# Optimization experiments

Measured on AMD Instinct MI355X. Metric: run time of the kernel, lower is better.

The kernel has to match this reference:

```python
import jax, jax.numpy as jnp
import numpy as np

N_NODES = 50000
N_EDGES = 300000
F_IN = 11
D = 256


def _gcn_conv(h, src, dst, deg_inv_sqrt, W, b, n):
    """PyG GCNConv: out = D^{-1/2} (A + I) D^{-1/2} (h W) + b.
    src/dst already include self-loops; deg_inv_sqrt precomputed."""
    norm = deg_inv_sqrt[src] * deg_inv_sqrt[dst]          # [E+N]
    hw = h @ W                                            # [N, D]
    msg = hw[src] * norm[:, None]                         # [E+N, D]
    out = jax.ops.segment_sum(msg, dst, num_segments=n)   # [N, D]
    return out + b


def setup_inputs() -> dict:
    key = jax.random.key(0)
    ks = jax.random.split(key, 8)
    x = jax.random.normal(ks[0], (N_NODES, F_IN), dtype=jnp.float32)
    edge_index = jax.random.randint(ks[1], (2, N_EDGES), 0, N_NODES, dtype=jnp.int32)
    s = 0.05
    W_embed = jax.random.normal(ks[2], (F_IN, D), dtype=jnp.float32) * s
    b_embed = jnp.zeros((D,), dtype=jnp.float32)
    W1 = jax.random.normal(ks[3], (D, D), dtype=jnp.float32) * s
    b1 = jnp.zeros((D,), dtype=jnp.float32)
    W2 = jax.random.normal(ks[4], (D, D), dtype=jnp.float32) * s
    b2 = jnp.zeros((D,), dtype=jnp.float32)
    return {"x": x, "edge_index": edge_index, "W_embed": W_embed, "b_embed": b_embed,
            "W1": W1, "b1": b1, "W2": W2, "b2": b2}


def reference(x, edge_index, W_embed, b_embed, W1, b1, W2, b2):
    n = x.shape[0]
    # add self-loops (PyG GCNConv default add_self_loops=True)
    loop = jnp.arange(n, dtype=edge_index.dtype)
    src = jnp.concatenate([edge_index[0], loop])
    dst = jnp.concatenate([edge_index[1], loop])
    # symmetric normalization: deg over target index with unit edge weights
    deg = jax.ops.segment_sum(jnp.ones(src.shape, dtype=x.dtype), dst, num_segments=n)
    deg_inv_sqrt = jnp.where(deg > 0, jax.lax.rsqrt(jnp.maximum(deg, 1e-12)), 0.0)

    h = jax.nn.relu(x @ W_embed + b_embed)                # embed + relu
    h = jax.nn.relu(_gcn_conv(h, src, dst, deg_inv_sqrt, W1, b1, n))
    h = _gcn_conv(h, src, dst, deg_inv_sqrt, W2, b2, n)
    return h
```

## Files before the change

### kernel.cpp

```cpp
#include <hip/hip_runtime.h>

#define N_NODES 50000
#define N_EDGES 300000
#define N_TOT   350000
#define D       256
#define MPAD    50048
#define SCAN_B  196

typedef __attribute__((ext_vector_type(8))) short bf16x8;
typedef __attribute__((ext_vector_type(4))) float f32x4;
typedef __attribute__((ext_vector_type(8))) unsigned short u16x8;

__device__ __forceinline__ float bf2f(unsigned short b) {
    union { unsigned u; float f; } v; v.u = ((unsigned)b) << 16; return v.f;
}
__device__ __forceinline__ unsigned short f2bf(float f) {
    union { float f; unsigned u; } v; v.f = f;
    unsigned u = v.u;
    unsigned r = (u + 0x7FFFu + ((u >> 16) & 1u)) >> 16;
    return (unsigned short)r;
}
__device__ __forceinline__ void g2lds16(const unsigned short* g, unsigned short* l) {
    __builtin_amdgcn_global_load_lds(
        (const __attribute__((address_space(1))) void*)g,
        (__attribute__((address_space(3))) void*)l, 16, 0, 0);
}

__global__ void hist_kernel(const int* __restrict__ ei, int* __restrict__ cnt) {
    int e = blockIdx.x * 256 + threadIdx.x;
    if (e >= N_TOT) return;
    int dst = (e < N_EDGES) ? ei[N_EDGES + e] : (e - N_EDGES);
    atomicAdd(&cnt[dst], 1);
}

__global__ void dis_kernel(const int* __restrict__ cnt, float* __restrict__ dis) {
    int i = blockIdx.x * 256 + threadIdx.x;
    if (i >= N_NODES) return;
    dis[i] = rsqrtf((float)cnt[i]);
}

__global__ void scan1_kernel(const int* __restrict__ cnt, int* __restrict__ locs,
                             int* __restrict__ bsum) {
    __shared__ int ws[4];
    int t = threadIdx.x, lane = t & 63, wv = t >> 6;
    int i = blockIdx.x * 256 + t;
    int v = (i < N_NODES) ? cnt[i] : 0;
    int s = v;
    #pragma unroll
    for (int d = 1; d < 64; d <<= 1) {
        int u = __shfl_up(s, d, 64);
        if (lane >= d) s += u;
    }
    if (lane == 63) ws[wv] = s;
    __syncthreads();
    int off = 0;
    #pragma unroll
    for (int k = 0; k < 4; ++k) if (k < wv) off += ws[k];
    s += off;
    if (i < N_NODES) locs[i] = s;
    if (t == 255) bsum[blockIdx.x] = s;
}
__global__ void scan2_kernel(int* __restrict__ bsum) {
    __shared__ int ws[4];
    int t = threadIdx.x, lane = t & 63, wv = t >> 6;
    int v = (t < SCAN_B) ? bsum[t] : 0;
    int s = v;
    #pragma unroll
    for (int d = 1; d < 64; d <<= 1) {
        int u = __shfl_up(s, d, 64);
        if (lane >= d) s += u;
    }
    if (lane == 63) ws[wv] = s;
    __syncthreads();
    int off = 0;
    #pragma unroll
    for (int k = 0; k < 4; ++k) if (k < wv) off += ws[k];
    s += off;
    if (t < SCAN_B) bsum[t] = s - v;
}
__global__ void scan3_kernel(const int* __restrict__ locs, const int* __restrict__ bsum,
                             int* __restrict__ rowptr) {
    int i = blockIdx.x * 256 + threadIdx.x;
    if (i == 0) rowptr[0] = 0;
    if (i < N_NODES) rowptr[i + 1] = locs[i] + bsum[i >> 8];
}

__global__ void fill_kernel(const int* __restrict__ ei, const int* __restrict__ rowptr,
                            int* __restrict__ fc, const float* __restrict__ dis,
                            int* __restrict__ esrc, float* __restrict__ enorm) {
    int e = blockIdx.x * 256 + threadIdx.x;
    if (e >= N_TOT) return;
    int src, dst;
    if (e < N_EDGES) { src = ei[e]; dst = ei[N_EDGES + e]; }
    else             { src = dst = e - N_EDGES; }
    int pos = rowptr[dst] + atomicAdd(&fc[dst], 1);
    esrc[pos]  = src;
    enorm[pos] = dis[src] * dis[dst];
}

__global__ void transpose_kernel(const float* __restrict__ W1,
                                 const float* __restrict__ W2,
                                 unsigned short* __restrict__ Wt1,
                                 unsigned short* __restrict__ Wt2) {
    int b = blockIdx.x, t = threadIdx.x;
    if (b < D) Wt1[b * D + t] = f2bf(W1[t * D + b]);
    else       Wt2[(b - D) * D + t] = f2bf(W2[t * D + (b - D)]);
}

__global__ void embed_kernel(const float* __restrict__ x,
                             const float* __restrict__ We,
                             const float* __restrict__ be,
                             unsigned short* __restrict__ hA) {
    int t = threadIdx.x;
    float w[11];
    #pragma unroll
    for (int k = 0; k < 11; ++k) w[k] = We[k * D + t];
    float b = be[t];
    int node0 = blockIdx.x * 8;
    #pragma unroll
    for (int ni = 0; ni < 8; ++ni) {
        int node = node0 + ni;
        float acc = 0.f;
        if (node < N_NODES) {
            acc = b;
            #pragma unroll
            for (int k = 0; k < 11; ++k) acc += x[node * 11 + k] * w[k];
            acc = fmaxf(acc, 0.f);
        }
        hA[(size_t)node * D + t] = f2bf(acc);
    }
}

__global__ __launch_bounds__(256) void gemm_kernel(const unsigned short* __restrict__ A,
                                                   const unsigned short* __restrict__ Bt,
                                                   unsigned short* __restrict__ C) {
    __shared__ unsigned short lA[128 * 32];
    __shared__ unsigned short lB[128 * 32];
    int t = threadIdx.x;
    int wv = t >> 6, lane = t & 63;
    int m0 = blockIdx.x * 128;
    int n0 = blockIdx.y * 128;
    int moff = (wv & 1) * 64, noff = (wv >> 1) * 64;
    int q = lane >> 4, r = lane & 15;

    int srow = t >> 2;
    int skof = (t & 3) * 8;

    const unsigned short* Ag0 = A  + (size_t)(m0 + srow) * D + skof;
    const unsigned short* Ag1 = Ag0 + (size_t)64 * D;
    const unsigned short* Bg0 = Bt + (size_t)(n0 + srow) * D + skof;
    const unsigned short* Bg1 = Bg0 + (size_t)64 * D;
    unsigned short* lA0 = lA + t * 8;
    unsigned short* lA1 = lA0 + 64 * 32;
    unsigned short* lB0 = lB + t * 8;
    unsigned short* lB1 = lB0 + 64 * 32;

    f32x4 acc[4][4] = {};
    for (int kk = 0; kk < D; kk += 32) {
        __syncthreads();
        g2lds16(Ag0 + kk, lA0);
        g2lds16(Ag1 + kk, lA1);
        g2lds16(Bg0 + kk, lB0);
        g2lds16(Bg1 + kk, lB1);
        __syncthreads();
        bf16x8 a[4], b[4];
        #pragma unroll
        for (int mt = 0; mt < 4; ++mt)
            a[mt] = *(const bf16x8*)(lA + (moff + mt * 16 + r) * 32 + q * 8);
        #pragma unroll
        for (int nt = 0; nt < 4; ++nt)
            b[nt] = *(const bf16x8*)(lB + (noff + nt * 16 + r) * 32 + q * 8);
        #pragma unroll
        for (int mt = 0; mt < 4; ++mt)
            #pragma unroll
            for (int nt = 0; nt < 4; ++nt)
                acc[mt][nt] = __builtin_amdgcn_mfma_f32_16x16x32_bf16(a[mt], b[nt], acc[mt][nt], 0, 0, 0);
    }
    #pragma unroll
    for (int mt = 0; mt < 4; ++mt)
        #pragma unroll
        for (int nt = 0; nt < 4; ++nt) {
            int col  = n0 + noff + nt * 16 + r;
            int rowb = m0 + moff + mt * 16 + q * 4;
            #pragma unroll
            for (int i = 0; i < 4; ++i)
                C[(size_t)(rowb + i) * D + col] = f2bf(acc[mt][nt][i]);
        }
}

__global__ __launch_bounds__(256) void agg_kernel(const unsigned short* __restrict__ hw,
                                                  const int* __restrict__ rowptr,
                                                  const int* __restrict__ esrc,
                                                  const float* __restrict__ enorm,
                                                  const float* __restrict__ bias,
                                                  unsigned short* __restrict__ out_bf,
                                                  float* __restrict__ out_f32,
                                                  int mode) {
    int wid  = threadIdx.x >> 6;
    int lane = threadIdx.x & 63;
    int node = blockIdx.x * 4 + wid;
    if (node >= N_NODES) return;
    int s0 = rowptr[node], s1 = rowptr[node + 1];
    int half = lane >> 5, hl = lane & 31;

    float acc[8] = {};
    for (int base = s0; base < s1; base += 64) {
        int ec = s1 - base; if (ec > 64) ec = 64;
        int   srcl = 0; float nml = 0.f;
        if (lane < ec) { srcl = esrc[base + lane]; nml = enorm[base + lane]; }
        int it = (ec + 1) >> 1;
        for (int i = 0; i < it; ++i) {
            int   e  = 2 * i + half;
            int   s  = __shfl(srcl, e, 64);
            float nm = __shfl(nml, e, 64);
            u16x8 hv = *(const u16x8*)(hw + (size_t)s * D + hl * 8);
            #pragma unroll
            for (int k = 0; k < 8; ++k) acc[k] += nm * bf2f(hv[k]);
        }
    }
    #pragma unroll
    for (int k = 0; k < 8; ++k) acc[k] += __shfl_xor(acc[k], 32, 64);

    if (lane < 32) {
        int c = hl * 8;
        float4 bv0 = *(const float4*)(bias + c);
        float4 bv1 = *(const float4*)(bias + c + 4);
        acc[0] += bv0.x; acc[1] += bv0.y; acc[2] += bv0.z; acc[3] += bv0.w;
        acc[4] += bv1.x; acc[5] += bv1.y; acc[6] += bv1.z; acc[7] += bv1.w;
        if (mode) {
            u16x8 ov;
            #pragma unroll
            for (int k = 0; k < 8; ++k) ov[k] = f2bf(fmaxf(acc[k], 0.f));
            *(u16x8*)(out_bf + (size_t)node * D + c) = ov;
        } else {
            float4 o0 = { acc[0], acc[1], acc[2], acc[3] };
            float4 o1 = { acc[4], acc[5], acc[6], acc[7] };
            *(float4*)(out_f32 + (size_t)node * D + c)     = o0;
            *(float4*)(out_f32 + (size_t)node * D + c + 4) = o1;
        }
    }
}

extern "C" void kernel_launch(void* const* d_in, const int* in_sizes, int n_in,
                              void* d_out, int out_size, void* d_ws, size_t ws_size,
                              hipStream_t stream) {
    const float* x  = (const float*)d_in[0];
    const int*   ei = (const int*)d_in[1];
    const float* We = (const float*)d_in[2];
    const float* be = (const float*)d_in[3];
    const float* W1 = (const float*)d_in[4];
    const float* b1 = (const float*)d_in[5];
    const float* W2 = (const float*)d_in[6];
    const float* b2 = (const float*)d_in[7];
    float* out = (float*)d_out;

    char* w = (char*)d_ws;
    auto alloc = [&](size_t bytes) {
        char* p = w;
        w += (bytes + 255) & ~(size_t)255;
        return p;
    };
    int*            cnt    = (int*)alloc((size_t)N_NODES * 4);
    int*            rowptr = (int*)alloc((size_t)(N_NODES + 1) * 4);
    int*            locs   = (int*)alloc((size_t)N_NODES * 4);
    int*            bsum   = (int*)alloc((size_t)SCAN_B * 4);
    float*          dis    = (float*)alloc((size_t)N_NODES * 4);
    int*            esrc   = (int*)alloc((size_t)N_TOT * 4);
    float*          enorm  = (float*)alloc((size_t)N_TOT * 4);
    unsigned short* Wt1    = (unsigned short*)alloc((size_t)D * D * 2);
    unsigned short* Wt2    = (unsigned short*)alloc((size_t)D * D * 2);
    unsigned short* hA     = (unsigned short*)alloc((size_t)MPAD * D * 2);
    unsigned short* hW     = (unsigned short*)alloc((size_t)MPAD * D * 2);

    hipMemsetAsync(cnt, 0, (size_t)N_NODES * 4, stream);
    hist_kernel<<<(N_TOT + 255) / 256, 256, 0, stream>>>(ei, cnt);
    dis_kernel<<<(N_NODES + 255) / 256, 256, 0, stream>>>(cnt, dis);
    scan1_kernel<<<SCAN_B, 256, 0, stream>>>(cnt, locs, bsum);
    scan2_kernel<<<1, 256, 0, stream>>>(bsum);
    scan3_kernel<<<SCAN_B, 256, 0, stream>>>(locs, bsum, rowptr);
    hipMemsetAsync(cnt, 0, (size_t)N_NODES * 4, stream);
    fill_kernel<<<(N_TOT + 255) / 256, 256, 0, stream>>>(ei, rowptr, cnt, dis, esrc, enorm);
    transpose_kernel<<<2 * D, 256, 0, stream>>>(W1, W2, Wt1, Wt2);

    embed_kernel<<<MPAD / 8, 256, 0, stream>>>(x, We, be, hA);

    dim3 ggrid(MPAD / 128, 2);
    gemm_kernel<<<ggrid, 256, 0, stream>>>(hA, Wt1, hW);
    agg_kernel<<<(N_NODES + 3) / 4, 256, 0, stream>>>(hW, rowptr, esrc, enorm, b1, hA, nullptr, 1);

    gemm_kernel<<<ggrid, 256, 0, stream>>>(hA, Wt2, hW);
    agg_kernel<<<(N_NODES + 3) / 4, 256, 0, stream>>>(hW, rowptr, esrc, enorm, b2, nullptr, out, 0);
}
```

Baseline: 242.0 us.

## Fuse graph setup, transpose and embed into one cooperative kernel with grid syncs

```diff
diff --git a/kernel.cpp b/kernel.cpp
--- a/kernel.cpp
+++ b/kernel.cpp
@@ -1,4 +1,7 @@
 #include <hip/hip_runtime.h>
+#include <hip/hip_cooperative_groups.h>
+
+namespace cg = cooperative_groups;
 
 #define N_NODES 50000
 #define N_EDGES 300000
@@ -6,6 +9,7 @@
 #define D       256
 #define MPAD    50048
 #define SCAN_B  196
+#define SETUP_GRID 512
 
 typedef __attribute__((ext_vector_type(8))) short bf16x8;
 typedef __attribute__((ext_vector_type(4))) float f32x4;
@@ -26,108 +30,109 @@
         (__attribute__((address_space(3))) void*)l, 16, 0, 0);
 }
 
-__global__ void hist_kernel(const int* __restrict__ ei, int* __restrict__ cnt) {
-    int e = blockIdx.x * 256 + threadIdx.x;
-    if (e >= N_TOT) return;
-    int dst = (e < N_EDGES) ? ei[N_EDGES + e] : (e - N_EDGES);
-    atomicAdd(&cnt[dst], 1);
-}
-
-__global__ void dis_kernel(const int* __restrict__ cnt, float* __restrict__ dis) {
-    int i = blockIdx.x * 256 + threadIdx.x;
-    if (i >= N_NODES) return;
-    dis[i] = rsqrtf((float)cnt[i]);
-}
-
-__global__ void scan1_kernel(const int* __restrict__ cnt, int* __restrict__ locs,
-                             int* __restrict__ bsum) {
+__global__ void __launch_bounds__(256) setup_kernel(
+        const float* __restrict__ x, const int* __restrict__ ei,
+        const float* __restrict__ We, const float* __restrict__ be,
+        const float* __restrict__ W1, const float* __restrict__ W2,
+        int* __restrict__ cnt, int* __restrict__ fc, float* __restrict__ dis,
+        int* __restrict__ locs, int* __restrict__ bsum, int* __restrict__ rowptr,
+        int* __restrict__ esrc, float* __restrict__ enorm,
+        unsigned short* __restrict__ Wt1, unsigned short* __restrict__ Wt2,
+        unsigned short* __restrict__ hA) {
+    cg::grid_group grid = cg::this_grid();
     __shared__ int ws[4];
-    int t = threadIdx.x, lane = t & 63, wv = t >> 6;
-    int i = blockIdx.x * 256 + t;
-    int v = (i < N_NODES) ? cnt[i] : 0;
-    int s = v;
-    #pragma unroll
-    for (int d = 1; d < 64; d <<= 1) {
-        int u = __shfl_up(s, d, 64);
-        if (lane >= d) s += u;
-    }
-    if (lane == 63) ws[wv] = s;
-    __syncthreads();
-    int off = 0;
-    #pragma unroll
-    for (int k = 0; k < 4; ++k) if (k < wv) off += ws[k];
-    s += off;
-    if (i < N_NODES) locs[i] = s;
-    if (t == 255) bsum[blockIdx.x] = s;
-}
-__global__ void scan2_kernel(int* __restrict__ bsum) {
-    __shared__ int ws[4];
-    int t = threadIdx.x, lane = t & 63, wv = t >> 6;
-    int v = (t < SCAN_B) ? bsum[t] : 0;
-    int s = v;
-    #pragma unroll
-    for (int d = 1; d < 64; d <<= 1) {
-        int u = __shfl_up(s, d, 64);
-        if (lane >= d) s += u;
-    }
-    if (lane == 63) ws[wv] = s;
-    __syncthreads();
-    int off = 0;
-    #pragma unroll
-    for (int k = 0; k < 4; ++k) if (k < wv) off += ws[k];
-    s += off;
-    if (t < SCAN_B) bsum[t] = s - v;
-}
-__global__ void scan3_kernel(const int* __restrict__ locs, const int* __restrict__ bsum,
-                             int* __restrict__ rowptr) {
-    int i = blockIdx.x * 256 + threadIdx.x;
-    if (i == 0) rowptr[0] = 0;
-    if (i < N_NODES) rowptr[i + 1] = locs[i] + bsum[i >> 8];
-}
-
-__global__ void fill_kernel(const int* __restrict__ ei, const int* __restrict__ rowptr,
-                            int* __restrict__ fc, const float* __restrict__ dis,
-                            int* __restrict__ esrc, float* __restrict__ enorm) {
-    int e = blockIdx.x * 256 + threadIdx.x;
-    if (e >= N_TOT) return;
-    int src, dst;
-    if (e < N_EDGES) { src = ei[e]; dst = ei[N_EDGES + e]; }
-    else             { src = dst = e - N_EDGES; }
-    int pos = rowptr[dst] + atomicAdd(&fc[dst], 1);
-    esrc[pos]  = src;
-    enorm[pos] = dis[src] * dis[dst];
-}
-
-__global__ void transpose_kernel(const float* __restrict__ W1,
-                                 const float* __restrict__ W2,
-                                 unsigned short* __restrict__ Wt1,
-                                 unsigned short* __restrict__ Wt2) {
-    int b = blockIdx.x, t = threadIdx.x;
-    if (b < D) Wt1[b * D + t] = f2bf(W1[t * D + b]);
-    else       Wt2[(b - D) * D + t] = f2bf(W2[t * D + (b - D)]);
-}
-
-__global__ void embed_kernel(const float* __restrict__ x,
-                             const float* __restrict__ We,
-                             const float* __restrict__ be,
-                             unsigned short* __restrict__ hA) {
     int t = threadIdx.x;
-    float w[11];
-    #pragma unroll
-    for (int k = 0; k < 11; ++k) w[k] = We[k * D + t];
-    float b = be[t];
-    int node0 = blockIdx.x * 8;
-    #pragma unroll
-    for (int ni = 0; ni < 8; ++ni) {
-        int node = node0 + ni;
-        float acc = 0.f;
-        if (node < N_NODES) {
-            acc = b;
-            #pragma unroll
-            for (int k = 0; k < 11; ++k) acc += x[node * 11 + k] * w[k];
-            acc = fmaxf(acc, 0.f);
-        }
-        hA[(size_t)node * D + t] = f2bf(acc);
+    int tid = blockIdx.x * 256 + t;
+    const int T = SETUP_GRID * 256;
+
+    for (int i = tid; i < N_NODES; i += T) { cnt[i] = 0; fc[i] = 0; }
+    for (int i = tid; i < 2 * D * D; i += T) {
+        int wsel = i >> 16, rem = i & 65535;
+        int tt = rem >> 8, b = rem & 255;
+        const float* W = wsel ? W2 : W1;
+        unsigned short* Wt = wsel ? Wt2 : Wt1;
+        Wt[b * D + tt] = f2bf(W[tt * D + b]);
+    }
+    {
+        float w[11];
+        #pragma unroll
+        for (int k = 0; k < 11; ++k) w[k] = We[k * D + t];
+        float bb = be[t];
+        for (int g = blockIdx.x; g < MPAD / 8; g += SETUP_GRID) {
+            #pragma unroll
+            for (int ni = 0; ni < 8; ++ni) {
+                int node = g * 8 + ni;
+                float acc = 0.f;
+                if (node < N_NODES) {
+                    acc = bb;
+                    #pragma unroll
+                    for (int k = 0; k < 11; ++k) acc += x[node * 11 + k] * w[k];
+                    acc = fmaxf(acc, 0.f);
+                }
+                hA[(size_t)node * D + t] = f2bf(acc);
+            }
+        }
+    }
+    grid.sync();
+
+    for (int e = tid; e < N_TOT; e += T) {
+        int dst = (e < N_EDGES) ? ei[N_EDGES + e] : (e - N_EDGES);
+        atomicAdd(&cnt[dst], 1);
+    }
+    grid.sync();
+
+    if (blockIdx.x < SCAN_B) {
+        int i = blockIdx.x * 256 + t;
+        int v = (i < N_NODES) ? cnt[i] : 0;
+        if (i < N_NODES) dis[i] = rsqrtf((float)v);
+        int lane = t & 63, wv = t >> 6;
+        int s = v;
+        #pragma unroll
+        for (int d = 1; d < 64; d <<= 1) {
+            int u = __shfl_up(s, d, 64);
+            if (lane >= d) s += u;
+        }
+        if (lane == 63) ws[wv] = s;
+        __syncthreads();
+        int off = 0;
+        #pragma unroll
+        for (int k = 0; k < 4; ++k) if (k < wv) off += ws[k];
+        s += off;
+        if (i < N_NODES) locs[i] = s;
+        if (t == 255) bsum[blockIdx.x] = s;
+    }
+    grid.sync();
+
+    if (blockIdx.x == 0) {
+        int v = (t < SCAN_B) ? bsum[t] : 0;
+        int lane = t & 63, wv = t >> 6;
+        int s = v;
+        #pragma unroll
+        for (int d = 1; d < 64; d <<= 1) {
+            int u = __shfl_up(s, d, 64);
+            if (lane >= d) s += u;
+        }
+        if (lane == 63) ws[wv] = s;
+        __syncthreads();
+        int off = 0;
+        #pragma unroll
+        for (int k = 0; k < 4; ++k) if (k < wv) off += ws[k];
+        s += off;
+        if (t < SCAN_B) bsum[t] = s - v;
+    }
+    grid.sync();
+
+    if (tid == 0) rowptr[0] = 0;
+    for (int i = tid; i < N_NODES; i += T)
+        rowptr[i + 1] = locs[i] + bsum[i >> 8];
+    for (int e = tid; e < N_TOT; e += T) {
+        int src, dst;
+        if (e < N_EDGES) { src = ei[e]; dst = ei[N_EDGES + e]; }
+        else             { src = dst = e - N_EDGES; }
+        int base = bsum[dst >> 8] + ((dst & 255) ? locs[dst - 1] : 0);
+        int pos = base + atomicAdd(&fc[dst], 1);
+        esrc[pos]  = src;
+        enorm[pos] = dis[src] * dis[dst];
     }
 }
 
@@ -261,6 +266,7 @@
         return p;
     };
     int*            cnt    = (int*)alloc((size_t)N_NODES * 4);
+    int*            fc     = (int*)alloc((size_t)N_NODES * 4);
     int*            rowptr = (int*)alloc((size_t)(N_NODES + 1) * 4);
     int*            locs   = (int*)alloc((size_t)N_NODES * 4);
     int*            bsum   = (int*)alloc((size_t)SCAN_B * 4);
@@ -272,17 +278,13 @@
     unsigned short* hA     = (unsigned short*)alloc((size_t)MPAD * D * 2);
     unsigned short* hW     = (unsigned short*)alloc((size_t)MPAD * D * 2);
 
-    hipMemsetAsync(cnt, 0, (size_t)N_NODES * 4, stream);
-    hist_kernel<<<(N_TOT + 255) / 256, 256, 0, stream>>>(ei, cnt);
-    dis_kernel<<<(N_NODES + 255) / 256, 256, 0, stream>>>(cnt, dis);
-    scan1_kernel<<<SCAN_B, 256, 0, stream>>>(cnt, locs, bsum);
-    scan2_kernel<<<1, 256, 0, stream>>>(bsum);
-    scan3_kernel<<<SCAN_B, 256, 0, stream>>>(locs, bsum, rowptr);
-    hipMemsetAsync(cnt, 0, (size_t)N_NODES * 4, stream);
-    fill_kernel<<<(N_TOT + 255) / 256, 256, 0, stream>>>(ei, rowptr, cnt, dis, esrc, enorm);
-    transpose_kernel<<<2 * D, 256, 0, stream>>>(W1, W2, Wt1, Wt2);
-
-    embed_kernel<<<MPAD / 8, 256, 0, stream>>>(x, We, be, hA);
+    void* args[] = { (void*)&x, (void*)&ei, (void*)&We, (void*)&be,
+                     (void*)&W1, (void*)&W2,
+                     (void*)&cnt, (void*)&fc, (void*)&dis, (void*)&locs,
+                     (void*)&bsum, (void*)&rowptr, (void*)&esrc, (void*)&enorm,
+                     (void*)&Wt1, (void*)&Wt2, (void*)&hA };
+    hipLaunchCooperativeKernel((const void*)setup_kernel, dim3(SETUP_GRID), dim3(256),
+                               args, 0, stream);
 
     dim3 ggrid(MPAD / 128, 2);
     gemm_kernel<<<ggrid, 256, 0, stream>>>(hA, Wt1, hW);
```

Measured after the change: 492.6 us. +103.5%, slower.
